# Kernel optimization log

Measured on AMD Instinct MI355X. Metric: run time of the kernel, lower is better.

Reference implementation:

```python
import jax, jax.numpy as jnp
import numpy as np

TT_IPS = (8, 16, 16)
TT_OPS = (16, 16, 16)
TT_RANKS = (1, 32, 32, 1)
BATCH = 4096


def setup_inputs() -> dict:
    key = jax.random.key(0)
    ks = jax.random.split(key, 6)
    ip0, ip1, ip2 = TT_IPS
    op0, op1, op2 = TT_OPS
    r1, r2 = TT_RANKS[1], TT_RANKS[2]
    # keras 'uniform' initializer: U(-0.05, 0.05)
    u = lambda k, s: jax.random.uniform(k, s, jnp.float32, -0.05, 0.05)
    return {
        "x": jax.random.normal(ks[0], (BATCH, ip0, ip1, ip2), jnp.float32),
        "core0": u(ks[1], (ip0, op0, r1)),
        "core1": u(ks[2], (r1, ip1, op1, r2)),
        "core2": u(ks[3], (r2, ip2, op2)),
        "bias": u(ks[4], (op0, op1, op2)),
    }


def reference(x, core0, core1, core2, bias):
    # Reconstruct dense weight via TT-core tensordot chain (as in the original).
    # core0: (i0, o0, r1); core1: (r1, i1, o1, r2); core2: (r2, i2, o2)
    w = jnp.tensordot(core0, core1, axes=[[-1], [0]])   # (i0, o0, i1, o1, r2)
    w = jnp.tensordot(w, core2, axes=[[-1], [0]])        # (i0, o0, i1, o1, i2, o2)
    # Contract input dims (1,2,3) of x with input dims (0,2,4) of w.
    out = jnp.tensordot(x, w, axes=[[1, 2, 3], [0, 2, 4]])  # (B, o0, o1, o2)
    return out + bias
```

## Files before the change

kernel.cpp:

```cpp
#include <hip/hip_runtime.h>
#include <hip/hip_bf16.h>
#include <stdint.h>


#define BATCH 4096
#define KIN   2048
#define NOUT  4096

typedef __bf16 bf16x8 __attribute__((ext_vector_type(8)));
typedef float  f32x4  __attribute__((ext_vector_type(4)));

__device__ __forceinline__ unsigned short f32_to_bf16_rne(float f) {
    union { float f; uint32_t u; } v; v.f = f;
    uint32_t u = v.u;
    u += 0x7fffu + ((u >> 16) & 1u);
    return (unsigned short)(u >> 16);
}

__global__ __launch_bounds__(256) void prep(
    const float* __restrict__ x,
    const float* __restrict__ core0,
    const float* __restrict__ core1,
    const float* __restrict__ core2,
    unsigned short* __restrict__ x2,
    unsigned short* __restrict__ wt)
{
    __shared__ float w01L[32 * 32];
    __shared__ float c2p[32 * 256];

    const int tid = threadIdx.x;
    const int blk = blockIdx.x;

    if (blk < 8192) {
        int g4 = blk * 256 + tid;
        f32x4 v = *(const f32x4*)&x[(size_t)g4 * 4];
        ushort4 h;
        h.x = f32_to_bf16_rne(v.x);
        h.y = f32_to_bf16_rne(v.y);
        h.z = f32_to_bf16_rne(v.z);
        h.w = f32_to_bf16_rne(v.w);
        *(ushort4*)&x2[(size_t)g4 * 4] = h;
        return;
    }

    const int b  = blk - 8192;
    const int rb = b * 32;
    const int row2  = rb >> 8;
    const int cbase = (rb & 255) * 32;

    {
        f32x4 acc4 = {0.f, 0.f, 0.f, 0.f};
        const float* c1p = core1 + cbase + tid * 4;
        const float* c0p = core0 + row2 * 32;
#pragma unroll
        for (int r1 = 0; r1 < 32; ++r1) {
            float a  = c0p[r1];
            f32x4 cv = *(const f32x4*)&c1p[(size_t)r1 * 8192];
            acc4 += a * cv;
        }
        *(f32x4*)&w01L[tid * 4] = acc4;
    }

#pragma unroll
    for (int i = 0; i < 8; ++i) {
        int fidx = tid + i * 256;
        int r2   = fidx >> 6;
        int cq   = fidx & 63;
        f32x4 v = *(const f32x4*)&core2[r2 * 256 + cq * 4];
#pragma unroll
        for (int j = 0; j < 4; ++j) {
            int cc = cq * 4 + j;
            int pc = (cc & 15) * 16 + (cc >> 4);
            c2p[r2 * 256 + pc] = v[j];
        }
    }
    __syncthreads();

    float acc[32];
#pragma unroll
    for (int r = 0; r < 32; ++r) acc[r] = 0.f;

#pragma unroll
    for (int q = 0; q < 8; ++q) {
        float cv0 = c2p[(4 * q + 0) * 256 + tid];
        float cv1 = c2p[(4 * q + 1) * 256 + tid];
        float cv2 = c2p[(4 * q + 2) * 256 + tid];
        float cv3 = c2p[(4 * q + 3) * 256 + tid];
#pragma unroll
        for (int r = 0; r < 32; ++r) {
            f32x4 w4 = *(const f32x4*)&w01L[r * 32 + q * 4];
            acc[r] += w4.x * cv0 + w4.y * cv1 + w4.z * cv2 + w4.w * cv3;
        }
    }

    const int i1base = (rb >> 4) & 15;
    const int o0     = (rb >> 8) & 15;
    const int i0     = rb >> 12;
    const int n0     = o0 * 256;
    const int k0     = i0 * 256 + i1base * 16;
    const int o2     = tid >> 4;
    const int i2     = tid & 15;

#pragma unroll
    for (int r = 0; r < 32; ++r) {
        int n = n0 + (r & 15) * 16 + o2;
        int k = k0 + (r >> 4) * 16 + i2;
        wt[(size_t)n * KIN + k] = f32_to_bf16_rne(acc[r]);
    }
}

__global__ __launch_bounds__(256, 2) void tt_gemm(
    const unsigned short* __restrict__ x2,
    const unsigned short* __restrict__ wt,
    const float* __restrict__ bias,
    float* __restrict__ out)
{
    __shared__ __align__(16) unsigned short lds_a[128 * 32];
    __shared__ __align__(16) unsigned short lds_b[128 * 32];

    const int tid  = threadIdx.x;
    const int lane = tid & 63;
    const int wid  = tid >> 6;
    const int wr   = wid >> 1;
    const int wc   = wid & 1;
    const int m0   = blockIdx.y * 128;
    const int n0   = blockIdx.x * 128;

    f32x4 acc[4][4] = {};

    const int seg0 = wid * 2 * 64 + lane;
    const int row0 = seg0 >> 2;
    const int cs0  = (seg0 & 3) * 8;
    const int seg1 = seg0 + 64;
    const int row1 = seg1 >> 2;
    const int cs1  = (seg1 & 3) * 8;

    for (int k0 = 0; k0 < KIN; k0 += 32) {
        const unsigned short* ga0 = x2 + (size_t)(m0 + row0) * KIN + k0 + cs0;
        const unsigned short* ga1 = x2 + (size_t)(m0 + row1) * KIN + k0 + cs1;
        const unsigned short* gb0 = wt + (size_t)(n0 + row0) * KIN + k0 + cs0;
        const unsigned short* gb1 = wt + (size_t)(n0 + row1) * KIN + k0 + cs1;

        __builtin_amdgcn_global_load_lds(
            (const __attribute__((address_space(1))) uint32_t*)ga0,
            (__attribute__((address_space(3))) uint32_t*)&lds_a[(wid * 2 + 0) * 512],
            16, 0, 0);
        __builtin_amdgcn_global_load_lds(
            (const __attribute__((address_space(1))) uint32_t*)ga1,
            (__attribute__((address_space(3))) uint32_t*)&lds_a[(wid * 2 + 1) * 512],
            16, 0, 0);
        __builtin_amdgcn_global_load_lds(
            (const __attribute__((address_space(1))) uint32_t*)gb0,
            (__attribute__((address_space(3))) uint32_t*)&lds_b[(wid * 2 + 0) * 512],
            16, 0, 0);
        __builtin_amdgcn_global_load_lds(
            (const __attribute__((address_space(1))) uint32_t*)gb1,
            (__attribute__((address_space(3))) uint32_t*)&lds_b[(wid * 2 + 1) * 512],
            16, 0, 0);

        __syncthreads();

        bf16x8 af[4], bf[4];
#pragma unroll
        for (int m = 0; m < 4; ++m)
            af[m] = *(const bf16x8*)&lds_a[(wr * 64 + m * 16 + (lane & 15)) * 32 + (lane >> 4) * 8];
#pragma unroll
        for (int n = 0; n < 4; ++n)
            bf[n] = *(const bf16x8*)&lds_b[(wc * 64 + n * 16 + (lane & 15)) * 32 + (lane >> 4) * 8];

#pragma unroll
        for (int m = 0; m < 4; ++m)
#pragma unroll
            for (int n = 0; n < 4; ++n)
                acc[m][n] = __builtin_amdgcn_mfma_f32_16x16x32_bf16(af[m], bf[n], acc[m][n], 0, 0, 0);

        __syncthreads();
    }

    const int colb = n0 + wc * 64 + (lane & 15);
#pragma unroll
    for (int n = 0; n < 4; ++n) {
        float bv = bias[colb + n * 16];
#pragma unroll
        for (int m = 0; m < 4; ++m) {
            int rbase = m0 + wr * 64 + m * 16 + (lane >> 4) * 4;
            f32x4 v = acc[m][n];
#pragma unroll
            for (int r = 0; r < 4; ++r)
                out[(size_t)(rbase + r) * NOUT + colb + n * 16] = v[r] + bv;
        }
    }
}

extern "C" void kernel_launch(void* const* d_in, const int* in_sizes, int n_in,
                              void* d_out, int out_size, void* d_ws, size_t ws_size,
                              hipStream_t stream) {
    const float* x     = (const float*)d_in[0];
    const float* core0 = (const float*)d_in[1];
    const float* core1 = (const float*)d_in[2];
    const float* core2 = (const float*)d_in[3];
    const float* bias  = (const float*)d_in[4];
    float* out = (float*)d_out;

    char* ws = (char*)d_ws;
    unsigned short* wt = (unsigned short*)ws;
    unsigned short* x2 = (unsigned short*)(ws + (16u << 20));

    prep   <<<8192 + 1024, 256, 0, stream>>>(x, core0, core1, core2, x2, wt);
    tt_gemm<<<dim3(32, 32), 256, 0, stream>>>(x2, wt, bias, out);
}
```

Baseline: 185.3 us.

## Replace GEMM with 256x256-tile double-buffered 8-wave pipelined kernel

Replaces the simple 128x128 single-buffered GEMM with a 256x256 tile kernel using 8 waves, a 64-wide K step, and double-buffered LDS (128KB dynamic). Global-to-LDS loads are interleaved with MFMA quadrants under explicit barriers, vmcnt waits and s_setprio, and an XOR swizzle is applied to LDS reads to avoid bank conflicts. The aim is to overlap memory traffic with compute and raise arithmetic intensity. The risks are lower occupancy, because 128KB of LDS per block allows at most one block per CU, and correctness sensitivity in the hand-tuned waitcnt schedule.

```diff
diff --git a/kernel.cpp b/kernel.cpp
--- a/kernel.cpp
+++ b/kernel.cpp
@@ -6,9 +6,12 @@
 #define BATCH 4096
 #define KIN   2048
 #define NOUT  4096
+#define NT    32
 
 typedef __bf16 bf16x8 __attribute__((ext_vector_type(8)));
 typedef float  f32x4  __attribute__((ext_vector_type(4)));
+typedef __attribute__((address_space(3))) uint32_t lds_u32;
+typedef const __attribute__((address_space(1))) uint32_t glb_u32;
 
 __device__ __forceinline__ unsigned short f32_to_bf16_rne(float f) {
     union { float f; uint32_t u; } v; v.f = f;
@@ -109,87 +112,132 @@
     }
 }
 
-__global__ __launch_bounds__(256, 2) void tt_gemm(
+
+__device__ __forceinline__ void readA8(const char* sm, int base, bf16x8 (&a)[8][2],
+                                       int MLO) {
+#pragma unroll
+    for (int m = 0; m < 4; ++m)
+#pragma unroll
+        for (int ks = 0; ks < 2; ++ks)
+            a[MLO + m][ks] = *(const bf16x8*)(sm + base + ((MLO + m) * 2 + ks) * 1024);
+}
+__device__ __forceinline__ void readB4(const char* sm, int base, bf16x8 (&b)[4][2],
+                                       int NLO) {
+#pragma unroll
+    for (int n = 0; n < 2; ++n)
+#pragma unroll
+        for (int ks = 0; ks < 2; ++ks)
+            b[NLO + n][ks] = *(const bf16x8*)(sm + base + ((NLO + n) * 2 + ks) * 1024);
+}
+__device__ __forceinline__ void quad(bf16x8 (&a)[8][2], bf16x8 (&b)[4][2],
+                                     f32x4 (&acc)[8][4], int MLO, int NLO) {
+#pragma unroll
+    for (int m = 0; m < 4; ++m)
+#pragma unroll
+        for (int n = 0; n < 2; ++n)
+#pragma unroll
+            for (int ks = 0; ks < 2; ++ks)
+                acc[MLO + m][NLO + n] = __builtin_amdgcn_mfma_f32_16x16x32_bf16(
+                    a[MLO + m][ks], b[NLO + n][ks], acc[MLO + m][NLO + n], 0, 0, 0);
+}
+
+#define BAR()   __builtin_amdgcn_s_barrier()
+#define LGKM0() asm volatile("s_waitcnt lgkmcnt(0)" ::: "memory")
+#define VM4()   do { asm volatile("s_waitcnt vmcnt(4)" ::: "memory"); \
+                     __builtin_amdgcn_sched_barrier(0); } while (0)
+#define PRIO1() __builtin_amdgcn_s_setprio(1)
+#define PRIO0() __builtin_amdgcn_s_setprio(0)
+
+__global__ __launch_bounds__(512, 2) void gemm8p(
     const unsigned short* __restrict__ x2,
     const unsigned short* __restrict__ wt,
     const float* __restrict__ bias,
     float* __restrict__ out)
 {
-    __shared__ __align__(16) unsigned short lds_a[128 * 32];
-    __shared__ __align__(16) unsigned short lds_b[128 * 32];
+    extern __shared__ char sm[];
 
     const int tid  = threadIdx.x;
     const int lane = tid & 63;
     const int wid  = tid >> 6;
-    const int wr   = wid >> 1;
-    const int wc   = wid & 1;
-    const int m0   = blockIdx.y * 128;
-    const int n0   = blockIdx.x * 128;
-
-    f32x4 acc[4][4] = {};
-
-    const int seg0 = wid * 2 * 64 + lane;
-    const int row0 = seg0 >> 2;
-    const int cs0  = (seg0 & 3) * 8;
-    const int seg1 = seg0 + 64;
-    const int row1 = seg1 >> 2;
-    const int cs1  = (seg1 & 3) * 8;
-
-    for (int k0 = 0; k0 < KIN; k0 += 32) {
-        const unsigned short* ga0 = x2 + (size_t)(m0 + row0) * KIN + k0 + cs0;
-        const unsigned short* ga1 = x2 + (size_t)(m0 + row1) * KIN + k0 + cs1;
-        const unsigned short* gb0 = wt + (size_t)(n0 + row0) * KIN + k0 + cs0;
-        const unsigned short* gb1 = wt + (size_t)(n0 + row1) * KIN + k0 + cs1;
-
-        __builtin_amdgcn_global_load_lds(
-            (const __attribute__((address_space(1))) uint32_t*)ga0,
-            (__attribute__((address_space(3))) uint32_t*)&lds_a[(wid * 2 + 0) * 512],
-            16, 0, 0);
-        __builtin_amdgcn_global_load_lds(
-            (const __attribute__((address_space(1))) uint32_t*)ga1,
-            (__attribute__((address_space(3))) uint32_t*)&lds_a[(wid * 2 + 1) * 512],
-            16, 0, 0);
-        __builtin_amdgcn_global_load_lds(
-            (const __attribute__((address_space(1))) uint32_t*)gb0,
-            (__attribute__((address_space(3))) uint32_t*)&lds_b[(wid * 2 + 0) * 512],
-            16, 0, 0);
-        __builtin_amdgcn_global_load_lds(
-            (const __attribute__((address_space(1))) uint32_t*)gb1,
-            (__attribute__((address_space(3))) uint32_t*)&lds_b[(wid * 2 + 1) * 512],
-            16, 0, 0);
-
-        __syncthreads();
-
-        bf16x8 af[4], bf[4];
-#pragma unroll
-        for (int m = 0; m < 4; ++m)
-            af[m] = *(const bf16x8*)&lds_a[(wr * 64 + m * 16 + (lane & 15)) * 32 + (lane >> 4) * 8];
-#pragma unroll
-        for (int n = 0; n < 4; ++n)
-            bf[n] = *(const bf16x8*)&lds_b[(wc * 64 + n * 16 + (lane & 15)) * 32 + (lane >> 4) * 8];
-
-#pragma unroll
-        for (int m = 0; m < 4; ++m)
-#pragma unroll
-            for (int n = 0; n < 4; ++n)
-                acc[m][n] = __builtin_amdgcn_mfma_f32_16x16x32_bf16(af[m], bf[n], acc[m][n], 0, 0, 0);
-
-        __syncthreads();
-    }
-
-    const int colb = n0 + wc * 64 + (lane & 15);
+    const int wm   = wid >> 2;
+    const int wn   = wid & 3;
+    const int m0   = blockIdx.y * 256;
+    const int n0g  = blockIdx.x * 256;
+
+    int xs = (lane & 15) * 64 + (lane >> 4) * 16;
+    xs ^= ((lane >> 3) & 1) << 5;
+    const int vaB = wm * 16384 + xs;
+    const int vbB = 65536 + (wn >> 1) * 16384 + (wn & 1) * 8192 + xs;
+
+    const int rr = lane >> 2;
+    const int cc = ((lane & 3) << 3) ^ ((lane & 32) >> 1);
+    const unsigned short* aSrc = x2 + (size_t)(m0 + wid * 16 + rr) * KIN + cc;
+    const unsigned short* bSrc = wt + (size_t)(n0g + wid * 16 + rr) * KIN + cc;
+    const int dstA = wid * 2048;
+    const int dstB = 65536 + wid * 2048;
+
+#define STAGE_A(b, h, kt) do { \
+    __builtin_amdgcn_global_load_lds((glb_u32*)(aSrc + (size_t)(h) * (128 * KIN) + (kt) * 64), \
+        (lds_u32*)(sm + ((b) * 2 + (h)) * 16384 + dstA), 16, 0, 0); \
+    __builtin_amdgcn_global_load_lds((glb_u32*)(aSrc + (size_t)(h) * (128 * KIN) + (kt) * 64 + 32), \
+        (lds_u32*)(sm + ((b) * 2 + (h)) * 16384 + dstA + 1024), 16, 0, 0); } while (0)
+#define STAGE_B(b, h, kt) do { \
+    __builtin_amdgcn_global_load_lds((glb_u32*)(bSrc + (size_t)(h) * (128 * KIN) + (kt) * 64), \
+        (lds_u32*)(sm + ((b) * 2 + (h)) * 16384 + dstB), 16, 0, 0); \
+    __builtin_amdgcn_global_load_lds((glb_u32*)(bSrc + (size_t)(h) * (128 * KIN) + (kt) * 64 + 32), \
+        (lds_u32*)(sm + ((b) * 2 + (h)) * 16384 + dstB + 1024), 16, 0, 0); } while (0)
+
+    f32x4 acc[8][4] = {};
+    bf16x8 a[8][2], b[4][2];
+
+    STAGE_A(0, 0, 0); STAGE_A(0, 1, 0);
+    STAGE_B(0, 0, 0); STAGE_B(0, 1, 0);
+    STAGE_A(1, 0, 1); STAGE_A(1, 1, 1);
+    asm volatile("s_waitcnt vmcnt(4)" ::: "memory");
+    __builtin_amdgcn_sched_barrier(0);
+    BAR();
+
+    for (int i = 0; i < NT / 2; ++i) {
+        const int t1 = 2 * i + 1;
+        const int p0 = (2 * i + 2) & (NT - 1);
+        const int p1 = (2 * i + 3) & (NT - 1);
+
+        readA8(sm, vaB + 0, a, 0); readB4(sm, vbB + 0, b, 0); STAGE_B(1, 0, t1);
+        BAR(); LGKM0(); PRIO1(); quad(a, b, acc, 0, 0); PRIO0(); BAR();
+        readA8(sm, vaB + 0, a, 4); STAGE_B(1, 1, t1);
+        BAR(); LGKM0(); PRIO1(); quad(a, b, acc, 4, 0); PRIO0(); BAR();
+        readB4(sm, vbB + 0, b, 2); STAGE_A(0, 0, p0);
+        BAR(); LGKM0(); PRIO1(); quad(a, b, acc, 0, 2); PRIO0(); BAR();
+        STAGE_A(0, 1, p0);
+        BAR(); PRIO1(); quad(a, b, acc, 4, 2); PRIO0(); VM4(); BAR();
+
+        readA8(sm, vaB + 32768, a, 0); readB4(sm, vbB + 32768, b, 0); STAGE_B(0, 0, p0);
+        BAR(); LGKM0(); PRIO1(); quad(a, b, acc, 0, 0); PRIO0(); BAR();
+        readA8(sm, vaB + 32768, a, 4); STAGE_B(0, 1, p0);
+        BAR(); LGKM0(); PRIO1(); quad(a, b, acc, 4, 0); PRIO0(); BAR();
+        readB4(sm, vbB + 32768, b, 2); STAGE_A(1, 0, p1);
+        BAR(); LGKM0(); PRIO1(); quad(a, b, acc, 0, 2); PRIO0(); BAR();
+        STAGE_A(1, 1, p1);
+        BAR(); PRIO1(); quad(a, b, acc, 4, 2); PRIO0(); VM4(); BAR();
+    }
+
+    asm volatile("s_waitcnt vmcnt(0)" ::: "memory");
+
 #pragma unroll
     for (int n = 0; n < 4; ++n) {
-        float bv = bias[colb + n * 16];
-#pragma unroll
-        for (int m = 0; m < 4; ++m) {
-            int rbase = m0 + wr * 64 + m * 16 + (lane >> 4) * 4;
+        const int col = n0g + wn * 64 + n * 16 + (lane & 15);
+        const float bv = bias[col];
+#pragma unroll
+        for (int m = 0; m < 8; ++m) {
+            const int rbase = m0 + wm * 128 + m * 16 + (lane >> 4) * 4;
             f32x4 v = acc[m][n];
 #pragma unroll
             for (int r = 0; r < 4; ++r)
-                out[(size_t)(rbase + r) * NOUT + colb + n * 16] = v[r] + bv;
-        }
-    }
+                out[(size_t)(rbase + r) * NOUT + col] = v[r] + bv;
+        }
+    }
+#undef STAGE_A
+#undef STAGE_B
 }
 
 extern "C" void kernel_launch(void* const* d_in, const int* in_sizes, int n_in,
@@ -206,6 +254,9 @@
     unsigned short* wt = (unsigned short*)ws;
     unsigned short* x2 = (unsigned short*)(ws + (16u << 20));
 
-    prep   <<<8192 + 1024, 256, 0, stream>>>(x, core0, core1, core2, x2, wt);
-    tt_gemm<<<dim3(32, 32), 256, 0, stream>>>(x2, wt, bias, out);
-}
+    hipFuncSetAttribute(reinterpret_cast<const void*>(&gemm8p),
+                        hipFuncAttributeMaxDynamicSharedMemorySize, 131072);
+
+    prep  <<<8192 + 1024, 256, 0, stream>>>(x, core0, core1, core2, x2, wt);
+    gemm8p<<<dim3(16, 16), 512, 131072, stream>>>(x2, wt, bias, out);
+}
```

New measurement: 170.6 us. -7.9%, faster.
